# Kernel tuning notes

Hardware: AMD Instinct MI355X
Metric: run time of the kernel (lower is better)

Reference implementation:

```python
import jax, jax.numpy as jnp
import numpy as np

N = 21  # nodes per graph (20 laser sectors + 1 robot node)
MAX_RANGE = 10.0
_bound = np.linspace(-np.pi / 2 - 0.03, np.pi / 2, 21, dtype=np.float32)[:-1]
_angles = _bound + np.float32(np.pi / 20)
ANGLE_FEAT = jnp.asarray(np.stack([np.sin(_angles), np.cos(_angles)], 1), dtype=jnp.float32)  # [20,2]


def _build_nodes(state24):
    # state24: [B,24] -> node features [B,21,7]
    B = state24.shape[0]
    laser = state24[:, :20, None] / MAX_RANGE                       # [B,20,1]
    angle = jnp.broadcast_to(ANGLE_FEAT[None], (B, 20, 2))          # [B,20,2]
    sector = jnp.concatenate([laser, angle, jnp.zeros((B, 20, 4), state24.dtype)], -1)  # [B,20,7]
    robot = jnp.concatenate([jnp.zeros((B, 1, 3), state24.dtype), state24[:, None, 20:]], -1)  # [B,1,7]
    return jnp.concatenate([sector, robot], axis=1)                 # [B,21,7]


def _gatv2(x, Wl, Wr, att, bias, heads, dim):
    # GATv2 over a fully-connected graph with self-loops (dense all-pairs).
    # e_ij = att . leaky_relu(Wl x_j + Wr x_i); alpha = softmax_j; out_i = sum_j alpha_ij (Wl x_j)
    B = x.shape[0]
    gl = (x @ Wl).reshape(B, N, heads, dim)  # source transform [B,j,H,D]
    gr = (x @ Wr).reshape(B, N, heads, dim)  # target transform [B,i,H,D]
    s = jax.nn.leaky_relu(gl[:, None] + gr[:, :, None], negative_slope=0.2)  # [B,i,j,H,D]
    e = jnp.einsum('bijhd,hd->bijh', s, att)                                  # [B,i,j,H]
    alpha = jax.nn.softmax(e, axis=2)                                          # softmax over sources j
    out = jnp.einsum('bijh,bjhd->bihd', alpha, gl).reshape(B, N, heads * dim)
    return out + bias


def setup_inputs() -> dict:
    key = jax.random.key(0)
    ks = jax.random.split(key, 16)
    r = lambda k, shape, s: (jax.random.normal(k, shape, dtype=jnp.float32) * s)
    B = 1024
    return {
        'state24': jax.random.normal(ks[0], (B, 24), dtype=jnp.float32),
        'Wl1': r(ks[1], (7, 256), 0.3), 'Wr1': r(ks[2], (7, 256), 0.3),
        'att1': r(ks[3], (4, 64), 0.1), 'b1': r(ks[4], (256,), 0.02),
        'Wl2': r(ks[5], (256, 64), 0.06), 'Wr2': r(ks[6], (256, 64), 0.06),
        'att2': r(ks[7], (1, 64), 0.1), 'b2': r(ks[8], (64,), 0.02),
        'fc1_w': r(ks[9], (64, 256), 0.12), 'fc1_b': r(ks[10], (256,), 0.02),
        'fc2_w': r(ks[11], (256, 256), 0.06), 'fc2_b': r(ks[12], (256,), 0.02),
        'fc3_w': r(ks[13], (256, 2), 0.06), 'fc3_b': r(ks[14], (2,), 0.02),
    }


def reference(state24, Wl1, Wr1, att1, b1, Wl2, Wr2, att2, b2,
              fc1_w, fc1_b, fc2_w, fc2_b, fc3_w, fc3_b):
    x = _build_nodes(state24)                               # [B,21,7]
    h = jax.nn.elu(_gatv2(x, Wl1, Wr1, att1, b1, 4, 64))    # [B,21,256]
    h = _gatv2(h, Wl2, Wr2, att2, b2, 1, 64)                # [B,21,64]
    nfv = jnp.mean(h, axis=1)                               # global_mean_pool -> [B,64]
    h = jax.nn.relu(nfv @ fc1_w + fc1_b)
    h = jax.nn.relu(h @ fc2_w + fc2_b)
    return jnp.tanh(h @ fc3_w + fc3_b)                      # [B,2]
```

## Files before the change

### kernel.cpp

```cpp
#include <hip/hip_runtime.h>
#include <hip/hip_fp16.h>
#include <math.h>

#define PI_D 3.141592653589793

typedef _Float16 h2 __attribute__((ext_vector_type(2)));
typedef _Float16 h4 __attribute__((ext_vector_type(4)));
typedef _Float16 h8 __attribute__((ext_vector_type(8)));
typedef unsigned short us8 __attribute__((ext_vector_type(8)));
typedef __fp16 f16v2 __attribute__((ext_vector_type(2)));
typedef __fp16 f16v8 __attribute__((ext_vector_type(8)));
typedef float f32x4 __attribute__((ext_vector_type(4)));

#define STR1 264
#define STR2H 72

#define SV(v, a, b) __builtin_shufflevector(v, v, a, b)

static __device__ __forceinline__ h2 pack_h2(float a, float b) {
    return __builtin_bit_cast(h2, __builtin_amdgcn_cvt_pkrtz(a, b));
}

static __device__ __forceinline__ float fdot2(h2 a, h2 b, float c) {
    return __builtin_amdgcn_fdot2(__builtin_bit_cast(f16v2, a),
                                  __builtin_bit_cast(f16v2, b), c, false);
}

static __device__ __forceinline__ h8 habs8(h8 x) {
    us8 u = __builtin_bit_cast(us8, x);
    us8 m = {0x7fff, 0x7fff, 0x7fff, 0x7fff, 0x7fff, 0x7fff, 0x7fff, 0x7fff};
    return __builtin_bit_cast(h8, (us8)(u & m));
}

static __device__ __forceinline__ f32x4 mfma16(h8 a, h8 b, f32x4 c) {
    return __builtin_amdgcn_mfma_f32_16x16x32_f16(
        __builtin_bit_cast(f16v8, a), __builtin_bit_cast(f16v8, b), c, 0, 0, 0);
}

static __device__ __forceinline__ void wave_fence() {
    asm volatile("" ::: "memory");
#if __has_builtin(__builtin_amdgcn_wave_barrier)
    __builtin_amdgcn_wave_barrier();
#endif
    asm volatile("" ::: "memory");
}

__global__ __launch_bounds__(256) void pack_weights_kernel(
    const float* __restrict__ Wl2, const float* __restrict__ Wr2,
    const float* __restrict__ fc1_w, const float* __restrict__ fc2_w,
    h8* __restrict__ ws)
{
    int idx = blockIdx.x * 256 + threadIdx.x;
    if (idx < 4096) {
        const float* W = idx < 2048 ? Wl2 : Wr2;
        int t = idx & 2047;
        int ntile = t >> 9, rem = t & 511;
        int kchunk = rem >> 6, lane = rem & 63;
        int n = ntile * 16 + (lane & 15);
        int k0 = kchunk * 32 + (lane >> 4) * 8;
        h8 o;
        #pragma unroll
        for (int j = 0; j < 8; ++j) o[j] = (_Float16)W[(k0 + j) * 64 + n];
        ws[idx] = o;
    } else if (idx < 6144) {
        int t = idx - 4096;
        int k2 = t >> 6, c = t & 63;
        h8 o;
        #pragma unroll
        for (int q = 0; q < 4; ++q) {
            o[2 * q]     = (_Float16)fc1_w[(2 * k2) * 256 + 4 * c + q];
            o[2 * q + 1] = (_Float16)fc1_w[(2 * k2 + 1) * 256 + 4 * c + q];
        }
        ws[idx] = o;
    } else {
        int t = idx - 6144;
        int k2 = t >> 6, c = t & 63;
        h8 o;
        #pragma unroll
        for (int q = 0; q < 4; ++q) {
            o[2 * q]     = (_Float16)fc2_w[(2 * k2) * 256 + 4 * c + q];
            o[2 * q + 1] = (_Float16)fc2_w[(2 * k2 + 1) * 256 + 4 * c + q];
        }
        ws[idx] = o;
    }
}

__global__ __launch_bounds__(256, 2) void actor_fused_kernel(
    const float* __restrict__ state24,
    const float* __restrict__ Wl1, const float* __restrict__ Wr1,
    const float* __restrict__ att1, const float* __restrict__ b1,
    const float* __restrict__ att2, const float* __restrict__ b2,
    const float* __restrict__ fc1_b, const float* __restrict__ fc2_b,
    const float* __restrict__ fc3_w, const float* __restrict__ fc3_b,
    const h8* __restrict__ wsL, const h8* __restrict__ wsR,
    const h8* __restrict__ wsF1, const h8* __restrict__ wsF2,
    float* __restrict__ out, int B)
{
    const int bix = blockIdx.x;
    const int tid = threadIdx.x;
    const int smp0 = 2 * bix;
    if (smp0 >= B) return;
    const int smp1 = (smp0 + 1 < B) ? smp0 + 1 : smp0;

    __shared__ float sinL[20], cosL[20], laserL[2][20], robotL[2][4];
    __shared__ __align__(16) h2 attLh[128];
    __shared__ __align__(16) h2 att2Lh[32];
    __shared__ __align__(16) _Float16 gr1h[2][22 * STR1];
    __shared__ __align__(16) union {
        struct { _Float16 gl1h[2][22 * STR1];
                 float ePf[2][128 * 24];
                 float uv[2][168]; } p1;
        struct { _Float16 gl2h[2][21 * STR2H];
                 _Float16 gr2h[2][21 * STR2H];
                 _Float16 gl2hT[2][64 * 32];
                 float e2[2][32 * 24];
                 float u2v2[2][42];
                 float red[2][4][256];
                 _Float16 nfvh[2][64]; _Float16 hah[2][256]; _Float16 hbh[2][256]; } p2;
    } U;

    if (tid < 20) {
        double step = (PI_D + 0.03) / 20.0;
        float bound = (float)(-PI_D / 2.0 - 0.03 + (double)tid * step);
        float ang = bound + (float)(PI_D / 20.0);
        sinL[tid] = sinf(ang);
        cosL[tid] = cosf(ang);
        laserL[0][tid] = state24[smp0 * 24 + tid] * 0.1f;
        laserL[1][tid] = state24[smp1 * 24 + tid] * 0.1f;
    }
    if (tid >= 32 && tid < 40) {
        int s = (tid - 32) >> 2, q = (tid - 32) & 3;
        robotL[s][q] = state24[(s ? smp1 : smp0) * 24 + 20 + q];
    }
    if (tid < 128) {
        float2 ap = ((const float2*)att1)[tid];
        attLh[tid] = pack_h2(0.4f * ap.x, 0.4f * ap.y);
    }
    if (tid >= 128 && tid < 160) {
        float2 ap = ((const float2*)att2)[tid - 128];
        att2Lh[tid - 128] = pack_h2(0.4f * ap.x, 0.4f * ap.y);
    }
    __syncthreads();

    {
        const int h = tid >> 6;
        const int lane = tid & 63;

        {
            const int cp = lane & 31;
            const int half = lane >> 5;
            const int d2 = h * 32 + cp;
            float2 wl[7], wr[7];
            #pragma unroll
            for (int k = 0; k < 7; k++) {
                wl[k] = ((const float2*)Wl1)[k * 128 + d2];
                wr[k] = ((const float2*)Wr1)[k * 128 + d2];
            }
            if (half == 0) {
                h2 zz2 = {};
                #pragma unroll
                for (int s = 0; s < 2; ++s) {
                    ((h2*)(U.p1.gl1h[s] + 21 * STR1))[d2] = zz2;
                    ((h2*)(gr1h[s] + 21 * STR1))[d2] = zz2;
                }
            }
            const int base = half * 11;
            #pragma unroll
            for (int nn = 0; nn < 11; ++nn) {
                int node = base + nn;
                if (node < 21) {
                    #pragma unroll
                    for (int s = 0; s < 2; ++s) {
                        float a0, a1, b0, b1v;
                        if (node < 20) {
                            float l = laserL[s][node], sv = sinL[node], c = cosL[node];
                            a0 = l * wl[0].x + sv * wl[1].x + c * wl[2].x;
                            a1 = l * wl[0].y + sv * wl[1].y + c * wl[2].y;
                            b0 = l * wr[0].x + sv * wr[1].x + c * wr[2].x;
                            b1v = l * wr[0].y + sv * wr[1].y + c * wr[2].y;
                        } else {
                            float r0 = robotL[s][0], r1 = robotL[s][1], r2 = robotL[s][2], r3 = robotL[s][3];
                            a0 = r0 * wl[3].x + r1 * wl[4].x + r2 * wl[5].x + r3 * wl[6].x;
                            a1 = r0 * wl[3].y + r1 * wl[4].y + r2 * wl[5].y + r3 * wl[6].y;
                            b0 = r0 * wr[3].x + r1 * wr[4].x + r2 * wr[5].x + r3 * wr[6].x;
                            b1v = r0 * wr[3].y + r1 * wr[4].y + r2 * wr[5].y + r3 * wr[6].y;
                        }
                        ((h2*)(U.p1.gl1h[s] + node * STR1))[d2] = pack_h2(a0, a1);
                        ((h2*)(gr1h[s] + node * STR1))[d2] = pack_h2(b0, b1v);
                    }
                }
            }
        }
        wave_fence();

        {
            h2 ar[32];
            #pragma unroll
            for (int q = 0; q < 32; ++q) ar[q] = attLh[h * 32 + q];

            const bool act = lane < 63;
            const int jn  = act ? lane % 21 : 0;
            const int seg = act ? lane / 21 : 0;

            #pragma unroll
            for (int s = 0; s < 2; ++s) {
                const h8* gA8 = (const h8*)(U.p1.gl1h[s] + jn * STR1 + h * 64);
                h8 gj[8];
                #pragma unroll
                for (int ch = 0; ch < 8; ++ch) gj[ch] = gA8[ch];

                if (act && seg == 0) {
                    float l0 = 0.f, l1 = 0.f;
                    #pragma unroll
                    for (int ch = 0; ch < 8; ++ch) {
                        l0 = fdot2(SV(gj[ch], 0, 1), ar[ch * 4 + 0], l0);
                        l1 = fdot2(SV(gj[ch], 2, 3), ar[ch * 4 + 1], l1);
                        l0 = fdot2(SV(gj[ch], 4, 5), ar[ch * 4 + 2], l0);
                        l1 = fdot2(SV(gj[ch], 6, 7), ar[ch * 4 + 3], l1);
                    }
                    U.p1.uv[s][h * 21 + jn] = l0 + l1;
                }

                #pragma unroll
                for (int t = 0; t < 7; ++t) {
                    const int i = seg * 7 + t;
                    const h8* gB8 = (const h8*)(gr1h[s] + i * STR1 + h * 64);
                    float m0 = 0.f, m1 = 0.f;
                    #pragma unroll
                    for (int ch = 0; ch < 8; ++ch) {
                        h8 x = gj[ch] + gB8[ch];
                        h8 ax = habs8(x);
                        m0 = fdot2(SV(ax, 0, 1), ar[ch * 4 + 0], m0);
                        m1 = fdot2(SV(ax, 2, 3), ar[ch * 4 + 1], m1);
                        m0 = fdot2(SV(ax, 4, 5), ar[ch * 4 + 2], m0);
                        m1 = fdot2(SV(ax, 6, 7), ar[ch * 4 + 3], m1);
                    }
                    if (act) U.p1.ePf[s][(h * 32 + i) * 24 + jn] = m0 + m1;
                }
            }

            if (lane < 42) {
                const int s = lane >= 21;
                const int idx = lane - s * 21;
                const h8* row8 = (const h8*)(gr1h[s] + idx * STR1 + h * 64);
                float l0 = 0.f, l1 = 0.f;
                #pragma unroll
                for (int ch = 0; ch < 8; ++ch) {
                    h8 g = row8[ch];
                    l0 = fdot2(SV(g, 0, 1), ar[ch * 4 + 0], l0);
                    l1 = fdot2(SV(g, 2, 3), ar[ch * 4 + 1], l1);
                    l0 = fdot2(SV(g, 4, 5), ar[ch * 4 + 2], l0);
                    l1 = fdot2(SV(g, 6, 7), ar[ch * 4 + 3], l1);
                }
                U.p1.uv[s][84 + h * 21 + idx] = l0 + l1;
            }
        }
        wave_fence();

        if (lane < 42) {
            int s = lane >= 21;
            int i = lane - s * 21;
            int r = h * 32 + i;
            float* row = U.p1.ePf[s] + r * 24;
            const float* uu = U.p1.uv[s] + h * 21;
            float vi = 1.5f * U.p1.uv[s][84 + h * 21 + i];
            float ebuf[21];
            float m = -1e30f;
            #pragma unroll
            for (int j = 0; j < 21; j++) {
                float e = row[j] + 1.5f * uu[j] + vi;
                ebuf[j] = e;
                m = fmaxf(m, e);
            }
            float sum = 0.f;
            #pragma unroll
            for (int j = 0; j < 21; j++) { float v = __expf(ebuf[j] - m); ebuf[j] = v; sum += v; }
            float rinv = 1.f / sum;
            h8* hp8 = (h8*)(U.p1.ePf[s]) + r * 6;
            h8 o0, o1, o2;
            #pragma unroll
            for (int q = 0; q < 8; ++q) o0[q] = (_Float16)(ebuf[q] * rinv);
            #pragma unroll
            for (int q = 0; q < 8; ++q) o1[q] = (_Float16)(ebuf[8 + q] * rinv);
            #pragma unroll
            for (int q = 0; q < 5; ++q) o2[q] = (_Float16)(ebuf[16 + q] * rinv);
            o2[5] = (_Float16)0.f; o2[6] = (_Float16)0.f; o2[7] = (_Float16)0.f;
            h8 zz = {};
            hp8[0] = o0; hp8[1] = o1; hp8[2] = o2;
            hp8[3] = zz; hp8[4] = zz; hp8[5] = zz;
        }
        {
            h8 zz = {};
            for (int z = lane; z < 132; z += 64) {
                int s = z >= 66;
                int zz2 = z - s * 66;
                int rr = zz2 / 6, slot = zz2 - rr * 6;
                ((h8*)U.p1.ePf[s])[(h * 32 + 21 + rr) * 6 + slot] = zz;
            }
        }
        wave_fence();

        {
            const int mcol = lane & 15;
            const int quad = lane >> 4;
            h8 A0s[2], A1s[2];
            #pragma unroll
            for (int s = 0; s < 2; ++s) {
                const h8* Af = (const h8*)U.p1.ePf[s];
                A0s[s] = Af[(h * 32 + mcol) * 6 + quad];
                A1s[s] = Af[(h * 32 + 16 + mcol) * 6 + quad];
            }
            int rowoff[8];
            #pragma unroll
            for (int jj = 0; jj < 8; ++jj) {
                int rr = quad * 8 + jj;
                rowoff[jj] = (rr > 21 ? 21 : rr) * STR1;
            }
            const int colbase = h * 64 + mcol;
            f32x4 z4 = {0.f, 0.f, 0.f, 0.f};
            #pragma unroll
            for (int t = 0; t < 4; ++t) {
                int col = colbase + t * 16;
                float bb = b1[col];
                #pragma unroll
                for (int s = 0; s < 2; ++s) {
                    h8 bv;
                    #pragma unroll
                    for (int jj = 0; jj < 8; ++jj) bv[jj] = U.p1.gl1h[s][rowoff[jj] + col];
                    f32x4 d0 = mfma16(A0s[s], bv, z4);
                    f32x4 d1 = mfma16(A1s[s], bv, z4);
                    #pragma unroll
                    for (int r = 0; r < 4; ++r) {
                        int n0 = quad * 4 + r;
                        float v = d0[r] + bb;
                        v = v > 0.f ? v : __expf(v) - 1.f;
                        gr1h[s][n0 * STR1 + col] = (_Float16)v;
                        int n1 = 16 + quad * 4 + r;
                        if (n1 < 21) {
                            float w2 = d1[r] + bb;
                            w2 = w2 > 0.f ? w2 : __expf(w2) - 1.f;
                            gr1h[s][n1 * STR1 + col] = (_Float16)w2;
                        }
                    }
                }
            }
        }
    }
    __syncthreads();

    {
        const int lane = tid & 63;
        const int w = tid >> 6;
        const int mrow = lane & 15;
        const int quad = lane >> 4;
        int rowA1 = 16 + mrow; if (rowA1 > 21) rowA1 = 21;
        const h8* bL = wsL + w * 512 + lane;
        const h8* bR = wsR + w * 512 + lane;
        f32x4 aL0[2], aL1[2], aR0[2], aR1[2];
        #pragma unroll
        for (int s = 0; s < 2; ++s) {
            aL0[s] = (f32x4){0.f, 0.f, 0.f, 0.f}; aL1[s] = (f32x4){0.f, 0.f, 0.f, 0.f};
            aR0[s] = (f32x4){0.f, 0.f, 0.f, 0.f}; aR1[s] = (f32x4){0.f, 0.f, 0.f, 0.f};
        }
        #pragma unroll
        for (int kc = 0; kc < 8; ++kc) {
            h8 BL = bL[kc * 64];
            h8 BR = bR[kc * 64];
            #pragma unroll
            for (int s = 0; s < 2; ++s) {
                h8 A0 = *(const h8*)(gr1h[s] + mrow * STR1 + quad * 8 + kc * 32);
                h8 A1 = *(const h8*)(gr1h[s] + rowA1 * STR1 + quad * 8 + kc * 32);
                aL0[s] = mfma16(A0, BL, aL0[s]);
                aL1[s] = mfma16(A1, BL, aL1[s]);
                aR0[s] = mfma16(A0, BR, aR0[s]);
                aR1[s] = mfma16(A1, BR, aR1[s]);
            }
        }
        const int col = w * 16 + mrow;
        #pragma unroll
        for (int s = 0; s < 2; ++s) {
            #pragma unroll
            for (int r = 0; r < 4; ++r) {
                int row0 = quad * 4 + r;
                U.p2.gl2h[s][row0 * STR2H + col] = (_Float16)aL0[s][r];
                U.p2.gr2h[s][row0 * STR2H + col] = (_Float16)aR0[s][r];
                int row1 = 16 + row0;
                if (row1 < 21) {
                    U.p2.gl2h[s][row1 * STR2H + col] = (_Float16)aL1[s][r];
                    U.p2.gr2h[s][row1 * STR2H + col] = (_Float16)aR1[s][r];
                }
            }
            h2 lo0 = pack_h2(aL0[s][0], aL0[s][1]);
            h2 hi0 = pack_h2(aL0[s][2], aL0[s][3]);
            h4 p0 = __builtin_shufflevector(lo0, hi0, 0, 1, 2, 3);
            *(h4*)(U.p2.gl2hT[s] + col * 32 + quad * 4) = p0;
            h2 lo1 = pack_h2(aL1[s][0], aL1[s][1]);
            h2 hi1 = pack_h2(aL1[s][2], aL1[s][3]);
            h4 p1 = __builtin_shufflevector(lo1, hi1, 0, 1, 2, 3);
            *(h4*)(U.p2.gl2hT[s] + col * 32 + 16 + quad * 4) = p1;
        }
    }
    __syncthreads();

    {
        h2 ar2[32];
        #pragma unroll
        for (int q = 0; q < 32; ++q) ar2[q] = att2Lh[q];

        const bool act = tid < 252;
        const int t0 = act ? tid : 0;
        const int jn = t0 % 21;
        const int sg = (t0 / 21) % 6;
        const int s  = t0 / 126;

        const h8* gA8 = (const h8*)(U.p2.gl2h[s] + jn * STR2H);
        h8 gj[8];
        #pragma unroll
        for (int ch = 0; ch < 8; ++ch) gj[ch] = gA8[ch];

        if (act && sg == 0) {
            float l0 = 0.f, l1 = 0.f;
            #pragma unroll
            for (int ch = 0; ch < 8; ++ch) {
                l0 = fdot2(SV(gj[ch], 0, 1), ar2[ch * 4 + 0], l0);
                l1 = fdot2(SV(gj[ch], 2, 3), ar2[ch * 4 + 1], l1);
                l0 = fdot2(SV(gj[ch], 4, 5), ar2[ch * 4 + 2], l0);
                l1 = fdot2(SV(gj[ch], 6, 7), ar2[ch * 4 + 3], l1);
            }
            U.p2.u2v2[s][jn] = l0 + l1;
        }

        #pragma unroll
        for (int tt = 0; tt < 4; ++tt) {
            const int i = sg * 4 + tt;
            const int ri = i < 21 ? i : 20;
            const h8* gB8 = (const h8*)(U.p2.gr2h[s] + ri * STR2H);
            float m0 = 0.f, m1 = 0.f;
            #pragma unroll
            for (int ch = 0; ch < 8; ++ch) {
                h8 x = gj[ch] + gB8[ch];
                h8 ax = habs8(x);
                m0 = fdot2(SV(ax, 0, 1), ar2[ch * 4 + 0], m0);
                m1 = fdot2(SV(ax, 2, 3), ar2[ch * 4 + 1], m1);
                m0 = fdot2(SV(ax, 4, 5), ar2[ch * 4 + 2], m0);
                m1 = fdot2(SV(ax, 6, 7), ar2[ch * 4 + 3], m1);
            }
            if (act && i < 21) U.p2.e2[s][i * 24 + jn] = m0 + m1;
        }

        if (tid < 42) {
            const int ss = tid >= 21;
            const int idx = tid - ss * 21;
            const h8* row8 = (const h8*)(U.p2.gr2h[ss] + idx * STR2H);
            float l0 = 0.f, l1 = 0.f;
            #pragma unroll
            for (int ch = 0; ch < 8; ++ch) {
                h8 g = row8[ch];
                l0 = fdot2(SV(g, 0, 1), ar2[ch * 4 + 0], l0);
                l1 = fdot2(SV(g, 2, 3), ar2[ch * 4 + 1], l1);
                l0 = fdot2(SV(g, 4, 5), ar2[ch * 4 + 2], l0);
                l1 = fdot2(SV(g, 6, 7), ar2[ch * 4 + 3], l1);
            }
            U.p2.u2v2[ss][21 + idx] = l0 + l1;
        }
    }
    __syncthreads();

    if (tid < 42) {
        int s = tid >= 21;
        int i = tid - s * 21;
        float* row = U.p2.e2[s] + i * 24;
        const float* uu = U.p2.u2v2[s];
        float vi = 1.5f * U.p2.u2v2[s][21 + i];
        float ebuf[21];
        float m = -1e30f;
        #pragma unroll
        for (int j = 0; j < 21; j++) {
            float e = row[j] + 1.5f * uu[j] + vi;
            ebuf[j] = e;
            m = fmaxf(m, e);
        }
        float sum = 0.f;
        #pragma unroll
        for (int j = 0; j < 21; j++) { float v = __expf(ebuf[j] - m); ebuf[j] = v; sum += v; }
        float rinv = 1.f / sum;
        h8* hp8 = (h8*)(U.p2.e2[s]) + i * 6;
        h8 o0, o1, o2;
        #pragma unroll
        for (int q = 0; q < 8; ++q) o0[q] = (_Float16)(ebuf[q] * rinv);
        #pragma unroll
        for (int q = 0; q < 8; ++q) o1[q] = (_Float16)(ebuf[8 + q] * rinv);
        #pragma unroll
        for (int q = 0; q < 5; ++q) o2[q] = (_Float16)(ebuf[16 + q] * rinv);
        o2[5] = (_Float16)0.f; o2[6] = (_Float16)0.f; o2[7] = (_Float16)0.f;
        h8 zz = {};
        hp8[0] = o0; hp8[1] = o1; hp8[2] = o2;
        hp8[3] = zz; hp8[4] = zz; hp8[5] = zz;
    } else if (tid < 174) {
        int z = tid - 42;
        int s = z >= 66;
        int zz2 = z - s * 66;
        int rr = zz2 / 6, slot = zz2 - rr * 6;
        h8 zz = {};
        ((h8*)U.p2.e2[s])[(21 + rr) * 6 + slot] = zz;
    }
    __syncthreads();

    {
        const int lane = tid & 63;
        const int w = tid >> 6;
        const int mcol = lane & 15;
        const int quad = lane >> 4;
        const int col = w * 16 + mcol;
        float bb = b2[col];
        f32x4 z4 = {0.f, 0.f, 0.f, 0.f};
        #pragma unroll
        for (int s = 0; s < 2; ++s) {
            const h8* Af2 = (const h8*)U.p2.e2[s];
            h8 A0 = Af2[mcol * 6 + quad];
            h8 A1 = Af2[(16 + mcol) * 6 + quad];
            h8 bv = *(const h8*)(U.p2.gl2hT[s] + col * 32 + quad * 8);
            f32x4 d0 = mfma16(A0, bv, z4);
            f32x4 d1 = mfma16(A1, bv, z4);
            float sum = (d0[0] + d0[1]) + (d0[2] + d0[3])
                      + (d1[0] + d1[1]) + (d1[2] + d1[3]);
            sum += __shfl_xor(sum, 16, 64);
            sum += __shfl_xor(sum, 32, 64);
            if (quad == 0) U.p2.nfvh[s][col] = (_Float16)(sum * (1.f / 21.f) + bb);
        }
    }
    __syncthreads();

    {
        int c = tid & 63, g = tid >> 6;
        float4 acc0 = {0.f, 0.f, 0.f, 0.f}, acc1 = {0.f, 0.f, 0.f, 0.f};
        #pragma unroll
        for (int kk = 0; kk < 8; ++kk) {
            int k2 = g * 8 + kk;
            h8 w = wsF1[k2 * 64 + c];
            h2 x0 = ((const h2*)U.p2.nfvh[0])[k2];
            h2 x1 = ((const h2*)U.p2.nfvh[1])[k2];
            acc0.x = fdot2(SV(w, 0, 1), x0, acc0.x);
            acc0.y = fdot2(SV(w, 2, 3), x0, acc0.y);
            acc0.z = fdot2(SV(w, 4, 5), x0, acc0.z);
            acc0.w = fdot2(SV(w, 6, 7), x0, acc0.w);
            acc1.x = fdot2(SV(w, 0, 1), x1, acc1.x);
            acc1.y = fdot2(SV(w, 2, 3), x1, acc1.y);
            acc1.z = fdot2(SV(w, 4, 5), x1, acc1.z);
            acc1.w = fdot2(SV(w, 6, 7), x1, acc1.w);
        }
        ((float4*)U.p2.red[0][g])[c] = acc0;
        ((float4*)U.p2.red[1][g])[c] = acc1;
    }
    __syncthreads();
    {
        float bb = fc1_b[tid];
        #pragma unroll
        for (int s = 0; s < 2; ++s) {
            float v = U.p2.red[s][0][tid] + U.p2.red[s][1][tid]
                    + U.p2.red[s][2][tid] + U.p2.red[s][3][tid] + bb;
            U.p2.hah[s][tid] = (_Float16)fmaxf(v, 0.f);
        }
    }
    __syncthreads();

    {
        int c = tid & 63, g = tid >> 6;
        const h8* ha0 = (const h8*)U.p2.hah[0];
        const h8* ha1 = (const h8*)U.p2.hah[1];
        float4 acc0 = {0.f, 0.f, 0.f, 0.f}, acc1 = {0.f, 0.f, 0.f, 0.f};
#define FC2_STEP(q, p)                                                          \
        {                                                                       \
            int k2 = g * 32 + (q) * 4 + (p);                                    \
            h8 w = wsF2[k2 * 64 + c];                                           \
            h2 x0 = __builtin_shufflevector(xa0, xa0, 2 * (p), 2 * (p) + 1);    \
            h2 x1 = __builtin_shufflevector(xa1, xa1, 2 * (p), 2 * (p) + 1);    \
            acc0.x = fdot2(SV(w, 0, 1), x0, acc0.x);                            \
            acc0.y = fdot2(SV(w, 2, 3), x0, acc0.y);                            \
            acc0.z = fdot2(SV(w, 4, 5), x0, acc0.z);                            \
            acc0.w = fdot2(SV(w, 6, 7), x0, acc0.w);                            \
            acc1.x = fdot2(SV(w, 0, 1), x1, acc1.x);                            \
            acc1.y = fdot2(SV(w, 2, 3), x1, acc1.y);                            \
            acc1.z = fdot2(SV(w, 4, 5), x1, acc1.z);                            \
            acc1.w = fdot2(SV(w, 6, 7), x1, acc1.w);                            \
        }
        #pragma unroll
        for (int q = 0; q < 8; ++q) {
            h8 xa0 = ha0[g * 8 + q];
            h8 xa1 = ha1[g * 8 + q];
            FC2_STEP(q, 0)
            FC2_STEP(q, 1)
            FC2_STEP(q, 2)
            FC2_STEP(q, 3)
        }
#undef FC2_STEP
        ((float4*)U.p2.red[0][g])[c] = acc0;
        ((float4*)U.p2.red[1][g])[c] = acc1;
    }
    __syncthreads();
    {
        float bb = fc2_b[tid];
        #pragma unroll
        for (int s = 0; s < 2; ++s) {
            float v = U.p2.red[s][0][tid] + U.p2.red[s][1][tid]
                    + U.p2.red[s][2][tid] + U.p2.red[s][3][tid] + bb;
            U.p2.hbh[s][tid] = (_Float16)fmaxf(v, 0.f);
        }
    }
    __syncthreads();

    {
        int g = tid >> 6;
        int o = g & 1, s = g >> 1;
        int l = tid & 63;
        float sum = 0.f;
        #pragma unroll
        for (int m = 0; m < 4; m++) {
            int k = l + 64 * m;
            sum = fmaf((float)U.p2.hbh[s][k], fc3_w[k * 2 + o], sum);
        }
        #pragma unroll
        for (int off = 32; off >= 1; off >>= 1) sum += __shfl_down(sum, off, 64);
        if (l == 0 && smp0 + s < B) out[(smp0 + s) * 2 + o] = tanhf(sum + fc3_b[o]);
    }
}

extern "C" void kernel_launch(void* const* d_in, const int* in_sizes, int n_in,
                              void* d_out, int out_size, void* d_ws, size_t ws_size,
                              hipStream_t stream) {
    const float* state24 = (const float*)d_in[0];
    const float* Wl1 = (const float*)d_in[1];
    const float* Wr1 = (const float*)d_in[2];
    const float* att1 = (const float*)d_in[3];
    const float* b1 = (const float*)d_in[4];
    const float* Wl2 = (const float*)d_in[5];
    const float* Wr2 = (const float*)d_in[6];
    const float* att2 = (const float*)d_in[7];
    const float* b2 = (const float*)d_in[8];
    const float* fc1_w = (const float*)d_in[9];
    const float* fc1_b = (const float*)d_in[10];
    const float* fc2_w = (const float*)d_in[11];
    const float* fc2_b = (const float*)d_in[12];
    const float* fc3_w = (const float*)d_in[13];
    const float* fc3_b = (const float*)d_in[14];
    float* out = (float*)d_out;

    h8* ws = (h8*)d_ws;
    const h8* wsL = ws;
    const h8* wsR = ws + 2048;
    const h8* wsF1 = ws + 4096;
    const h8* wsF2 = ws + 6144;

    pack_weights_kernel<<<56, 256, 0, stream>>>(Wl2, Wr2, fc1_w, fc2_w, ws);

    int B = in_sizes[0] / 24;
    int nb = (B + 1) / 2;
    actor_fused_kernel<<<nb, 256, 0, stream>>>(
        state24, Wl1, Wr1, att1, b1, att2, b2,
        fc1_b, fc2_b, fc3_w, fc3_b,
        wsL, wsR, wsF1, wsF2, out, B);
}
```

Baseline: 112.7 us.

## Process one sample per block instead of two to raise occupancy

```diff
diff --git a/kernel.cpp b/kernel.cpp
--- a/kernel.cpp
+++ b/kernel.cpp
@@ -85,7 +85,7 @@
     }
 }
 
-__global__ __launch_bounds__(256, 2) void actor_fused_kernel(
+__global__ __launch_bounds__(256, 4) void actor_fused_kernel(
     const float* __restrict__ state24,
     const float* __restrict__ Wl1, const float* __restrict__ Wr1,
     const float* __restrict__ att1, const float* __restrict__ b1,
@@ -96,27 +96,24 @@
     const h8* __restrict__ wsF1, const h8* __restrict__ wsF2,
     float* __restrict__ out, int B)
 {
-    const int bix = blockIdx.x;
+    const int smp = blockIdx.x;
     const int tid = threadIdx.x;
-    const int smp0 = 2 * bix;
-    if (smp0 >= B) return;
-    const int smp1 = (smp0 + 1 < B) ? smp0 + 1 : smp0;
-
-    __shared__ float sinL[20], cosL[20], laserL[2][20], robotL[2][4];
+
+    __shared__ float sinL[20], cosL[20], laserL[20], robotL[4];
     __shared__ __align__(16) h2 attLh[128];
     __shared__ __align__(16) h2 att2Lh[32];
-    __shared__ __align__(16) _Float16 gr1h[2][22 * STR1];
+    __shared__ __align__(16) _Float16 gr1h[22 * STR1];
     __shared__ __align__(16) union {
-        struct { _Float16 gl1h[2][22 * STR1];
-                 float ePf[2][128 * 24];
-                 float uv[2][168]; } p1;
-        struct { _Float16 gl2h[2][21 * STR2H];
-                 _Float16 gr2h[2][21 * STR2H];
-                 _Float16 gl2hT[2][64 * 32];
-                 float e2[2][32 * 24];
-                 float u2v2[2][42];
-                 float red[2][4][256];
-                 _Float16 nfvh[2][64]; _Float16 hah[2][256]; _Float16 hbh[2][256]; } p2;
+        struct { _Float16 gl1h[22 * STR1];
+                 float ePf[128 * 24];
+                 float uv[168]; } p1;
+        struct { _Float16 gl2h[21 * STR2H];
+                 _Float16 gr2h[21 * STR2H];
+                 _Float16 gl2hT[64 * 32];
+                 float e2[32 * 24];
+                 float u2v2[42];
+                 float red[4][256];
+                 _Float16 nfvh[64]; _Float16 hah[256]; _Float16 hbh[256]; } p2;
     } U;
 
     if (tid < 20) {
@@ -125,12 +122,11 @@
         float ang = bound + (float)(PI_D / 20.0);
         sinL[tid] = sinf(ang);
         cosL[tid] = cosf(ang);
-        laserL[0][tid] = state24[smp0 * 24 + tid] * 0.1f;
-        laserL[1][tid] = state24[smp1 * 24 + tid] * 0.1f;
-    }
-    if (tid >= 32 && tid < 40) {
-        int s = (tid - 32) >> 2, q = (tid - 32) & 3;
-        robotL[s][q] = state24[(s ? smp1 : smp0) * 24 + 20 + q];
+        laserL[tid] = state24[smp * 24 + tid] * 0.1f;
+    }
+    if (tid >= 32 && tid < 36) {
+        int q = tid - 32;
+        robotL[q] = state24[smp * 24 + 20 + q];
     }
     if (tid < 128) {
         float2 ap = ((const float2*)att1)[tid];
@@ -158,36 +154,30 @@
             }
             if (half == 0) {
                 h2 zz2 = {};
-                #pragma unroll
-                for (int s = 0; s < 2; ++s) {
-                    ((h2*)(U.p1.gl1h[s] + 21 * STR1))[d2] = zz2;
-                    ((h2*)(gr1h[s] + 21 * STR1))[d2] = zz2;
-                }
+                ((h2*)(U.p1.gl1h + 21 * STR1))[d2] = zz2;
+                ((h2*)(gr1h + 21 * STR1))[d2] = zz2;
             }
             const int base = half * 11;
             #pragma unroll
             for (int nn = 0; nn < 11; ++nn) {
                 int node = base + nn;
                 if (node < 21) {
-                    #pragma unroll
-                    for (int s = 0; s < 2; ++s) {
-                        float a0, a1, b0, b1v;
-                        if (node < 20) {
-                            float l = laserL[s][node], sv = sinL[node], c = cosL[node];
-                            a0 = l * wl[0].x + sv * wl[1].x + c * wl[2].x;
-                            a1 = l * wl[0].y + sv * wl[1].y + c * wl[2].y;
-                            b0 = l * wr[0].x + sv * wr[1].x + c * wr[2].x;
-                            b1v = l * wr[0].y + sv * wr[1].y + c * wr[2].y;
-                        } else {
-                            float r0 = robotL[s][0], r1 = robotL[s][1], r2 = robotL[s][2], r3 = robotL[s][3];
-                            a0 = r0 * wl[3].x + r1 * wl[4].x + r2 * wl[5].x + r3 * wl[6].x;
-                            a1 = r0 * wl[3].y + r1 * wl[4].y + r2 * wl[5].y + r3 * wl[6].y;
-                            b0 = r0 * wr[3].x + r1 * wr[4].x + r2 * wr[5].x + r3 * wr[6].x;
-                            b1v = r0 * wr[3].y + r1 * wr[4].y + r2 * wr[5].y + r3 * wr[6].y;
-                        }
-                        ((h2*)(U.p1.gl1h[s] + node * STR1))[d2] = pack_h2(a0, a1);
-                        ((h2*)(gr1h[s] + node * STR1))[d2] = pack_h2(b0, b1v);
+                    float a0, a1, b0, b1v;
+                    if (node < 20) {
+                        float l = laserL[node], sv = sinL[node], c = cosL[node];
+                        a0 = l * wl[0].x + sv * wl[1].x + c * wl[2].x;
+                        a1 = l * wl[0].y + sv * wl[1].y + c * wl[2].y;
+                        b0 = l * wr[0].x + sv * wr[1].x + c * wr[2].x;
+                        b1v = l * wr[0].y + sv * wr[1].y + c * wr[2].y;
+                    } else {
+                        float r0 = robotL[0], r1 = robotL[1], r2 = robotL[2], r3 = robotL[3];
+                        a0 = r0 * wl[3].x + r1 * wl[4].x + r2 * wl[5].x + r3 * wl[6].x;
+                        a1 = r0 * wl[3].y + r1 * wl[4].y + r2 * wl[5].y + r3 * wl[6].y;
+                        b0 = r0 * wr[3].x + r1 * wr[4].x + r2 * wr[5].x + r3 * wr[6].x;
+                        b1v = r0 * wr[3].y + r1 * wr[4].y + r2 * wr[5].y + r3 * wr[6].y;
                     }
+                    ((h2*)(U.p1.gl1h + node * STR1))[d2] = pack_h2(a0, a1);
+                    ((h2*)(gr1h + node * STR1))[d2] = pack_h2(b0, b1v);
                 }
             }
         }
@@ -202,47 +192,42 @@
             const int jn  = act ? lane % 21 : 0;
             const int seg = act ? lane / 21 : 0;
 
-            #pragma unroll
-            for (int s = 0; s < 2; ++s) {
-                const h8* gA8 = (const h8*)(U.p1.gl1h[s] + jn * STR1 + h * 64);
-                h8 gj[8];
+            const h8* gA8 = (const h8*)(U.p1.gl1h + jn * STR1 + h * 64);
+            h8 gj[8];
+            #pragma unroll
+            for (int ch = 0; ch < 8; ++ch) gj[ch] = gA8[ch];
+
+            if (act && seg == 0) {
+                float l0 = 0.f, l1 = 0.f;
                 #pragma unroll
-                for (int ch = 0; ch < 8; ++ch) gj[ch] = gA8[ch];
-
-                if (act && seg == 0) {
-                    float l0 = 0.f, l1 = 0.f;
-                    #pragma unroll
-                    for (int ch = 0; ch < 8; ++ch) {
-                        l0 = fdot2(SV(gj[ch], 0, 1), ar[ch * 4 + 0], l0);
-                        l1 = fdot2(SV(gj[ch], 2, 3), ar[ch * 4 + 1], l1);
-                        l0 = fdot2(SV(gj[ch], 4, 5), ar[ch * 4 + 2], l0);
-                        l1 = fdot2(SV(gj[ch], 6, 7), ar[ch * 4 + 3], l1);
-                    }
-                    U.p1.uv[s][h * 21 + jn] = l0 + l1;
+                for (int ch = 0; ch < 8; ++ch) {
+                    l0 = fdot2(SV(gj[ch], 0, 1), ar[ch * 4 + 0], l0);
+                    l1 = fdot2(SV(gj[ch], 2, 3), ar[ch * 4 + 1], l1);
+                    l0 = fdot2(SV(gj[ch], 4, 5), ar[ch * 4 + 2], l0);
+                    l1 = fdot2(SV(gj[ch], 6, 7), ar[ch * 4 + 3], l1);
                 }
-
+                U.p1.uv[h * 21 + jn] = l0 + l1;
+            }
+
+            #pragma unroll
+            for (int t = 0; t < 7; ++t) {
+                const int i = seg * 7 + t;
+                const h8* gB8 = (const h8*)(gr1h + i * STR1 + h * 64);
+                float m0 = 0.f, m1 = 0.f;
                 #pragma unroll
-                for (int t = 0; t < 7; ++t) {
-                    const int i = seg * 7 + t;
-                    const h8* gB8 = (const h8*)(gr1h[s] + i * STR1 + h * 64);
-                    float m0 = 0.f, m1 = 0.f;
-                    #pragma unroll
-                    for (int ch = 0; ch < 8; ++ch) {
-                        h8 x = gj[ch] + gB8[ch];
-                        h8 ax = habs8(x);
-                        m0 = fdot2(SV(ax, 0, 1), ar[ch * 4 + 0], m0);
-                        m1 = fdot2(SV(ax, 2, 3), ar[ch * 4 + 1], m1);
-                        m0 = fdot2(SV(ax, 4, 5), ar[ch * 4 + 2], m0);
-                        m1 = fdot2(SV(ax, 6, 7), ar[ch * 4 + 3], m1);
-                    }
-                    if (act) U.p1.ePf[s][(h * 32 + i) * 24 + jn] = m0 + m1;
+                for (int ch = 0; ch < 8; ++ch) {
+                    h8 x = gj[ch] + gB8[ch];
+                    h8 ax = habs8(x);
+                    m0 = fdot2(SV(ax, 0, 1), ar[ch * 4 + 0], m0);
+                    m1 = fdot2(SV(ax, 2, 3), ar[ch * 4 + 1], m1);
+                    m0 = fdot2(SV(ax, 4, 5), ar[ch * 4 + 2], m0);
+                    m1 = fdot2(SV(ax, 6, 7), ar[ch * 4 + 3], m1);
                 }
-            }
-
-            if (lane < 42) {
-                const int s = lane >= 21;
-                const int idx = lane - s * 21;
-                const h8* row8 = (const h8*)(gr1h[s] + idx * STR1 + h * 64);
+                if (act) U.p1.ePf[(h * 32 + i) * 24 + jn] = m0 + m1;
+            }
+
+            if (lane < 21) {
+                const h8* row8 = (const h8*)(gr1h + lane * STR1 + h * 64);
                 float l0 = 0.f, l1 = 0.f;
                 #pragma unroll
                 for (int ch = 0; ch < 8; ++ch) {
@@ -252,18 +237,17 @@
                     l0 = fdot2(SV(g, 4, 5), ar[ch * 4 + 2], l0);
                     l1 = fdot2(SV(g, 6, 7), ar[ch * 4 + 3], l1);
                 }
-                U.p1.uv[s][84 + h * 21 + idx] = l0 + l1;
+                U.p1.uv[84 + h * 21 + lane] = l0 + l1;
             }
         }
         wave_fence();
 
-        if (lane < 42) {
-            int s = lane >= 21;
-            int i = lane - s * 21;
+        if (lane < 21) {
+            int i = lane;
             int r = h * 32 + i;
-            float* row = U.p1.ePf[s] + r * 24;
-            const float* uu = U.p1.uv[s] + h * 21;
-            float vi = 1.5f * U.p1.uv[s][84 + h * 21 + i];
+            float* row = U.p1.ePf + r * 24;
+            const float* uu = U.p1.uv + h * 21;
+            float vi = 1.5f * U.p1.uv[84 + h * 21 + i];
             float ebuf[21];
             float m = -1e30f;
             #pragma unroll
@@ -276,7 +260,7 @@
             #pragma unroll
             for (int j = 0; j < 21; j++) { float v = __expf(ebuf[j] - m); ebuf[j] = v; sum += v; }
             float rinv = 1.f / sum;
-            h8* hp8 = (h8*)(U.p1.ePf[s]) + r * 6;
+            h8* hp8 = (h8*)(U.p1.ePf) + r * 6;
             h8 o0, o1, o2;
             #pragma unroll
             for (int q = 0; q < 8; ++q) o0[q] = (_Float16)(ebuf[q] * rinv);
@@ -291,11 +275,9 @@
         }
         {
             h8 zz = {};
-            for (int z = lane; z < 132; z += 64) {
-                int s = z >= 66;
-                int zz2 = z - s * 66;
-                int rr = zz2 / 6, slot = zz2 - rr * 6;
-                ((h8*)U.p1.ePf[s])[(h * 32 + 21 + rr) * 6 + slot] = zz;
+            for (int z = lane; z < 66; z += 64) {
+                int rr = z / 6, slot = z - rr * 6;
+                ((h8*)U.p1.ePf)[(h * 32 + 21 + rr) * 6 + slot] = zz;
             }
         }
         wave_fence();
@@ -303,13 +285,9 @@
         {
             const int mcol = lane & 15;
             const int quad = lane >> 4;
-            h8 A0s[2], A1s[2];
-            #pragma unroll
-            for (int s = 0; s < 2; ++s) {
-                const h8* Af = (const h8*)U.p1.ePf[s];
-                A0s[s] = Af[(h * 32 + mcol) * 6 + quad];
-                A1s[s] = Af[(h * 32 + 16 + mcol) * 6 + quad];
-            }
+            const h8* Af = (const h8*)U.p1.ePf;
+            h8 A0 = Af[(h * 32 + mcol) * 6 + quad];
+            h8 A1 = Af[(h * 32 + 16 + mcol) * 6 + quad];
             int rowoff[8];
             #pragma unroll
             for (int jj = 0; jj < 8; ++jj) {
@@ -322,25 +300,22 @@
             for (int t = 0; t < 4; ++t) {
                 int col = colbase + t * 16;
                 float bb = b1[col];
+                h8 bv;
                 #pragma unroll
-                for (int s = 0; s < 2; ++s) {
-                    h8 bv;
-                    #pragma unroll
-                    for (int jj = 0; jj < 8; ++jj) bv[jj] = U.p1.gl1h[s][rowoff[jj] + col];
-                    f32x4 d0 = mfma16(A0s[s], bv, z4);
-                    f32x4 d1 = mfma16(A1s[s], bv, z4);
-                    #pragma unroll
-                    for (int r = 0; r < 4; ++r) {
-                        int n0 = quad * 4 + r;
-                        float v = d0[r] + bb;
-                        v = v > 0.f ? v : __expf(v) - 1.f;
-                        gr1h[s][n0 * STR1 + col] = (_Float16)v;
-                        int n1 = 16 + quad * 4 + r;
-                        if (n1 < 21) {
-                            float w2 = d1[r] + bb;
-                            w2 = w2 > 0.f ? w2 : __expf(w2) - 1.f;
-                            gr1h[s][n1 * STR1 + col] = (_Float16)w2;
-                        }
+                for (int jj = 0; jj < 8; ++jj) bv[jj] = U.p1.gl1h[rowoff[jj] + col];
+                f32x4 d0 = mfma16(A0, bv, z4);
+                f32x4 d1 = mfma16(A1, bv, z4);
+                #pragma unroll
+                for (int r = 0; r < 4; ++r) {
+                    int n0 = quad * 4 + r;
+                    float v = d0[r] + bb;
+                    v = v > 0.f ? v : __expf(v) - 1.f;
+                    gr1h[n0 * STR1 + col] = (_Float16)v;
+                    int n1 = 16 + quad * 4 + r;
+                    if (n1 < 21) {
+                        float w2 = d1[r] + bb;
+                        w2 = w2 > 0.f ? w2 : __expf(w2) - 1.f;
+                        gr1h[n1 * STR1 + col] = (_Float16)w2;
                     }
                 }
             }
@@ -356,49 +331,39 @@
         int rowA1 = 16 + mrow; if (rowA1 > 21) rowA1 = 21;
         const h8* bL = wsL + w * 512 + lane;
         const h8* bR = wsR + w * 512 + lane;
-        f32x4 aL0[2], aL1[2], aR0[2], aR1[2];
-        #pragma unroll
-        for (int s = 0; s < 2; ++s) {
-            aL0[s] = (f32x4){0.f, 0.f, 0.f, 0.f}; aL1[s] = (f32x4){0.f, 0.f, 0.f, 0.f};
-            aR0[s] = (f32x4){0.f, 0.f, 0.f, 0.f}; aR1[s] = (f32x4){0.f, 0.f, 0.f, 0.f};
-        }
+        f32x4 aL0 = {0.f, 0.f, 0.f, 0.f}, aL1 = {0.f, 0.f, 0.f, 0.f};
+        f32x4 aR0 = {0.f, 0.f, 0.f, 0.f}, aR1 = {0.f, 0.f, 0.f, 0.f};
         #pragma unroll
         for (int kc = 0; kc < 8; ++kc) {
             h8 BL = bL[kc * 64];
             h8 BR = bR[kc * 64];
-            #pragma unroll
-            for (int s = 0; s < 2; ++s) {
-                h8 A0 = *(const h8*)(gr1h[s] + mrow * STR1 + quad * 8 + kc * 32);
-                h8 A1 = *(const h8*)(gr1h[s] + rowA1 * STR1 + quad * 8 + kc * 32);
-                aL0[s] = mfma16(A0, BL, aL0[s]);
-                aL1[s] = mfma16(A1, BL, aL1[s]);
-                aR0[s] = mfma16(A0, BR, aR0[s]);
-                aR1[s] = mfma16(A1, BR, aR1[s]);
-            }
+            h8 A0 = *(const h8*)(gr1h + mrow * STR1 + quad * 8 + kc * 32);
+            h8 A1 = *(const h8*)(gr1h + rowA1 * STR1 + quad * 8 + kc * 32);
+            aL0 = mfma16(A0, BL, aL0);
+            aL1 = mfma16(A1, BL, aL1);
+            aR0 = mfma16(A0, BR, aR0);
+            aR1 = mfma16(A1, BR, aR1);
         }
         const int col = w * 16 + mrow;
         #pragma unroll
-        for (int s = 0; s < 2; ++s) {
-            #pragma unroll
-            for (int r = 0; r < 4; ++r) {
-                int row0 = quad * 4 + r;
-                U.p2.gl2h[s][row0 * STR2H + col] = (_Float16)aL0[s][r];
-                U.p2.gr2h[s][row0 * STR2H + col] = (_Float16)aR0[s][r];
-                int row1 = 16 + row0;
-                if (row1 < 21) {
-                    U.p2.gl2h[s][row1 * STR2H + col] = (_Float16)aL1[s][r];
-                    U.p2.gr2h[s][row1 * STR2H + col] = (_Float16)aR1[s][r];
-                }
-            }
-            h2 lo0 = pack_h2(aL0[s][0], aL0[s][1]);
-            h2 hi0 = pack_h2(aL0[s][2], aL0[s][3]);
-            h4 p0 = __builtin_shufflevector(lo0, hi0, 0, 1, 2, 3);
-            *(h4*)(U.p2.gl2hT[s] + col * 32 + quad * 4) = p0;
-            h2 lo1 = pack_h2(aL1[s][0], aL1[s][1]);
-            h2 hi1 = pack_h2(aL1[s][2], aL1[s][3]);
-            h4 p1 = __builtin_shufflevector(lo1, hi1, 0, 1, 2, 3);
-            *(h4*)(U.p2.gl2hT[s] + col * 32 + 16 + quad * 4) = p1;
-        }
+        for (int r = 0; r < 4; ++r) {
+            int row0 = quad * 4 + r;
+            U.p2.gl2h[row0 * STR2H + col] = (_Float16)aL0[r];
+            U.p2.gr2h[row0 * STR2H + col] = (_Float16)aR0[r];
+            int row1 = 16 + row0;
+            if (row1 < 21) {
+                U.p2.gl2h[row1 * STR2H + col] = (_Float16)aL1[r];
+                U.p2.gr2h[row1 * STR2H + col] = (_Float16)aR1[r];
+            }
+        }
+        h2 lo0 = pack_h2(aL0[0], aL0[1]);
+        h2 hi0 = pack_h2(aL0[2], aL0[3]);
+        h4 p0 = __builtin_shufflevector(lo0, hi0, 0, 1, 2, 3);
+        *(h4*)(U.p2.gl2hT + col * 32 + quad * 4) = p0;
+        h2 lo1 = pack_h2(aL1[0], aL1[1]);
+        h2 hi1 = pack_h2(aL1[2], aL1[3]);
+        h4 p1 = __builtin_shufflevector(lo1, hi1, 0, 1, 2, 3);
+        *(h4*)(U.p2.gl2hT + col * 32 + 16 + quad * 4) = p1;
     }
     __syncthreads();
 
@@ -410,10 +375,9 @@
         const bool act = tid < 252;
         const int t0 = act ? tid : 0;
         const int jn = t0 % 21;
-        const int sg = (t0 / 21) % 6;
-        const int s  = t0 / 126;
-
-        const h8* gA8 = (const h8*)(U.p2.gl2h[s] + jn * STR2H);
+        const int sg = t0 / 21;
+
+        const h8* gA8 = (const h8*)(U.p2.gl2h + jn * STR2H);
         h8 gj[8];
         #pragma unroll
         for (int ch = 0; ch < 8; ++ch) gj[ch] = gA8[ch];
@@ -427,31 +391,29 @@
                 l0 = fdot2(SV(gj[ch], 4, 5), ar2[ch * 4 + 2], l0);
                 l1 = fdot2(SV(gj[ch], 6, 7), ar2[ch * 4 + 3], l1);
             }
-            U.p2.u2v2[s][jn] = l0 + l1;
-        }
-
-        #pragma unroll
-        for (int tt = 0; tt < 4; ++tt) {
-            const int i = sg * 4 + tt;
-            const int ri = i < 21 ? i : 20;
-            const h8* gB8 = (const h8*)(U.p2.gr2h[s] + ri * STR2H);
-            float m0 = 0.f, m1 = 0.f;
-            #pragma unroll
-            for (int ch = 0; ch < 8; ++ch) {
-                h8 x = gj[ch] + gB8[ch];
-                h8 ax = habs8(x);
-                m0 = fdot2(SV(ax, 0, 1), ar2[ch * 4 + 0], m0);
-                m1 = fdot2(SV(ax, 2, 3), ar2[ch * 4 + 1], m1);
-                m0 = fdot2(SV(ax, 4, 5), ar2[ch * 4 + 2], m0);
-                m1 = fdot2(SV(ax, 6, 7), ar2[ch * 4 + 3], m1);
-            }
-            if (act && i < 21) U.p2.e2[s][i * 24 + jn] = m0 + m1;
-        }
-
-        if (tid < 42) {
-            const int ss = tid >= 21;
-            const int idx = tid - ss * 21;
-            const h8* row8 = (const h8*)(U.p2.gr2h[ss] + idx * STR2H);
+            U.p2.u2v2[jn] = l0 + l1;
+        }
+
+        if (sg < 11) {
+            #pragma unroll
+            for (int tt = 0; tt < 2; ++tt) {
+                const int i = sg * 2 + tt;
+                const int ri = i < 21 ? i : 20;
+                const h8* gB8 = (const h8*)(U.p2.gr2h + ri * STR2H);
+                float m0 = 0.f, m1 = 0.f;
+                #pragma unroll
+                for (int ch = 0; ch < 8; ++ch) {
+                    h8 x = gj[ch] + gB8[ch];
+                    h8 ax = habs8(x);
+                    m0 = fdot2(SV(ax, 0, 1), ar2[ch * 4 + 0], m0);
+                    m1 = fdot2(SV(ax, 2, 3), ar2[ch * 4 + 1], m1);
+                    m0 = fdot2(SV(ax, 4, 5), ar2[ch * 4 + 2], m0);
+                    m1 = fdot2(SV(ax, 6, 7), ar2[ch * 4 + 3], m1);
+                }
+                if (act && i < 21) U.p2.e2[i * 24 + jn] = m0 + m1;
+            }
+        } else if (act) {
+            const h8* row8 = (const h8*)(U.p2.gr2h + jn * STR2H);
             float l0 = 0.f, l1 = 0.f;
             #pragma unroll
             for (int ch = 0; ch < 8; ++ch) {
@@ -461,17 +423,16 @@
                 l0 = fdot2(SV(g, 4, 5), ar2[ch * 4 + 2], l0);
                 l1 = fdot2(SV(g, 6, 7), ar2[ch * 4 + 3], l1);
             }
-            U.p2.u2v2[ss][21 + idx] = l0 + l1;
-        }
-    }
-    __syncthreads();
-
-    if (tid < 42) {
-        int s = tid >= 21;
-        int i = tid - s * 21;
-        float* row = U.p2.e2[s] + i * 24;
-        const float* uu = U.p2.u2v2[s];
-        float vi = 1.5f * U.p2.u2v2[s][21 + i];
+            U.p2.u2v2[21 + jn] = l0 + l1;
+        }
+    }
+    __syncthreads();
+
+    if (tid < 21) {
+        int i = tid;
+        float* row = U.p2.e2 + i * 24;
+        const float* uu = U.p2.u2v2;
+        float vi = 1.5f * U.p2.u2v2[21 + i];
         float ebuf[21];
         float m = -1e30f;
         #pragma unroll
@@ -484,7 +445,7 @@
         #pragma unroll
         for (int j = 0; j < 21; j++) { float v = __expf(ebuf[j] - m); ebuf[j] = v; sum += v; }
         float rinv = 1.f / sum;
-        h8* hp8 = (h8*)(U.p2.e2[s]) + i * 6;
+        h8* hp8 = (h8*)(U.p2.e2) + i * 6;
         h8 o0, o1, o2;
         #pragma unroll
         for (int q = 0; q < 8; ++q) o0[q] = (_Float16)(ebuf[q] * rinv);
@@ -496,13 +457,11 @@
         h8 zz = {};
         hp8[0] = o0; hp8[1] = o1; hp8[2] = o2;
         hp8[3] = zz; hp8[4] = zz; hp8[5] = zz;
-    } else if (tid < 174) {
-        int z = tid - 42;
-        int s = z >= 66;
-        int zz2 = z - s * 66;
-        int rr = zz2 / 6, slot = zz2 - rr * 6;
+    } else if (tid < 87) {
+        int z = tid - 21;
+        int rr = z / 6, slot = z - rr * 6;
         h8 zz = {};
-        ((h8*)U.p2.e2[s])[(21 + rr) * 6 + slot] = zz;
+        ((h8*)U.p2.e2)[(21 + rr) * 6 + slot] = zz;
     }
     __syncthreads();
 
@@ -514,114 +473,93 @@
         const int col = w * 16 + mcol;
         float bb = b2[col];
         f32x4 z4 = {0.f, 0.f, 0.f, 0.f};
-        #pragma unroll
-        for (int s = 0; s < 2; ++s) {
-            const h8* Af2 = (const h8*)U.p2.e2[s];
-            h8 A0 = Af2[mcol * 6 + quad];
-            h8 A1 = Af2[(16 + mcol) * 6 + quad];
-            h8 bv = *(const h8*)(U.p2.gl2hT[s] + col * 32 + quad * 8);
-            f32x4 d0 = mfma16(A0, bv, z4);
-            f32x4 d1 = mfma16(A1, bv, z4);
-            float sum = (d0[0] + d0[1]) + (d0[2] + d0[3])
-                      + (d1[0] + d1[1]) + (d1[2] + d1[3]);
-            sum += __shfl_xor(sum, 16, 64);
-            sum += __shfl_xor(sum, 32, 64);
-            if (quad == 0) U.p2.nfvh[s][col] = (_Float16)(sum * (1.f / 21.f) + bb);
-        }
+        const h8* Af2 = (const h8*)U.p2.e2;
+        h8 A0 = Af2[mcol * 6 + quad];
+        h8 A1 = Af2[(16 + mcol) * 6 + quad];
+        h8 bv = *(const h8*)(U.p2.gl2hT + col * 32 + quad * 8);
+        f32x4 d0 = mfma16(A0, bv, z4);
+        f32x4 d1 = mfma16(A1, bv, z4);
+        float sum = (d0[0] + d0[1]) + (d0[2] + d0[3])
+                  + (d1[0] + d1[1]) + (d1[2] + d1[3]);
+        sum += __shfl_xor(sum, 16, 64);
+        sum += __shfl_xor(sum, 32, 64);
+        if (quad == 0) U.p2.nfvh[col] = (_Float16)(sum * (1.f / 21.f) + bb);
     }
     __syncthreads();
 
     {
         int c = tid & 63, g = tid >> 6;
-        float4 acc0 = {0.f, 0.f, 0.f, 0.f}, acc1 = {0.f, 0.f, 0.f, 0.f};
+        float4 acc = {0.f, 0.f, 0.f, 0.f};
         #pragma unroll
         for (int kk = 0; kk < 8; ++kk) {
             int k2 = g * 8 + kk;
             h8 w = wsF1[k2 * 64 + c];
-            h2 x0 = ((const h2*)U.p2.nfvh[0])[k2];
-            h2 x1 = ((const h2*)U.p2.nfvh[1])[k2];
-            acc0.x = fdot2(SV(w, 0, 1), x0, acc0.x);
-            acc0.y = fdot2(SV(w, 2, 3), x0, acc0.y);
-            acc0.z = fdot2(SV(w, 4, 5), x0, acc0.z);
-            acc0.w = fdot2(SV(w, 6, 7), x0, acc0.w);
-            acc1.x = fdot2(SV(w, 0, 1), x1, acc1.x);
-            acc1.y = fdot2(SV(w, 2, 3), x1, acc1.y);
-            acc1.z = fdot2(SV(w, 4, 5), x1, acc1.z);
-            acc1.w = fdot2(SV(w, 6, 7), x1, acc1.w);
-        }
-        ((float4*)U.p2.red[0][g])[c] = acc0;
-        ((float4*)U.p2.red[1][g])[c] = acc1;
+            h2 x = ((const h2*)U.p2.nfvh)[k2];
+            acc.x = fdot2(SV(w, 0, 1), x, acc.x);
+            acc.y = fdot2(SV(w, 2, 3), x, acc.y);
+            acc.z = fdot2(SV(w, 4, 5), x, acc.z);
+            acc.w = fdot2(SV(w, 6, 7), x, acc.w);
+        }
+        ((float4*)U.p2.red[g])[c] = acc;
     }
     __syncthreads();
     {
         float bb = fc1_b[tid];
-        #pragma unroll
-        for (int s = 0; s < 2; ++s) {
-            float v = U.p2.red[s][0][tid] + U.p2.red[s][1][tid]
-                    + U.p2.red[s][2][tid] + U.p2.red[s][3][tid] + bb;
-            U.p2.hah[s][tid] = (_Float16)fmaxf(v, 0.f);
-        }
+        float v = U.p2.red[0][tid] + U.p2.red[1][tid]
+                + U.p2.red[2][tid] + U.p2.red[3][tid] + bb;
+        U.p2.hah[tid] = (_Float16)fmaxf(v, 0.f);
     }
     __syncthreads();
 
     {
         int c = tid & 63, g = tid >> 6;
-        const h8* ha0 = (const h8*)U.p2.hah[0];
-        const h8* ha1 = (const h8*)U.p2.hah[1];
-        float4 acc0 = {0.f, 0.f, 0.f, 0.f}, acc1 = {0.f, 0.f, 0.f, 0.f};
+        const h8* ha = (const h8*)U.p2.hah;
+        float4 acc = {0.f, 0.f, 0.f, 0.f};
 #define FC2_STEP(q, p)                                                          \
         {                                                                       \
             int k2 = g * 32 + (q) * 4 + (p);                                    \
             h8 w = wsF2[k2 * 64 + c];                                           \
-            h2 x0 = __builtin_shufflevector(xa0, xa0, 2 * (p), 2 * (p) + 1);    \
-            h2 x1 = __builtin_shufflevector(xa1, xa1, 2 * (p), 2 * (p) + 1);    \
-            acc0.x = fdot2(SV(w, 0, 1), x0, acc0.x);                            \
-            acc0.y = fdot2(SV(w, 2, 3), x0, acc0.y);                            \
-            acc0.z = fdot2(SV(w, 4, 5), x0, acc0.z);                            \
-            acc0.w = fdot2(SV(w, 6, 7), x0, acc0.w);                            \
-            acc1.x = fdot2(SV(w, 0, 1), x1, acc1.x);                            \
-            acc1.y = fdot2(SV(w, 2, 3), x1, acc1.y);                            \
-            acc1.z = fdot2(SV(w, 4, 5), x1, acc1.z);                            \
-            acc1.w = fdot2(SV(w, 6, 7), x1, acc1.w);                            \
+            h2 x = __builtin_shufflevector(xa, xa, 2 * (p), 2 * (p) + 1);       \
+            acc.x = fdot2(SV(w, 0, 1), x, acc.x);                               \
+            acc.y = fdot2(SV(w, 2, 3), x, acc.y);                               \
+            acc.z = fdot2(SV(w, 4, 5), x, acc.z);                               \
+            acc.w = fdot2(SV(w, 6, 7), x, acc.w);                               \
         }
         #pragma unroll
         for (int q = 0; q < 8; ++q) {
-            h8 xa0 = ha0[g * 8 + q];
-            h8 xa1 = ha1[g * 8 + q];
+            h8 xa = ha[g * 8 + q];
             FC2_STEP(q, 0)
             FC2_STEP(q, 1)
             FC2_STEP(q, 2)
             FC2_STEP(q, 3)
         }
 #undef FC2_STEP
-        ((float4*)U.p2.red[0][g])[c] = acc0;
-        ((float4*)U.p2.red[1][g])[c] = acc1;
+        ((float4*)U.p2.red[g])[c] = acc;
     }
     __syncthreads();
     {
         float bb = fc2_b[tid];
-        #pragma unroll
-        for (int s = 0; s < 2; ++s) {
-            float v = U.p2.red[s][0][tid] + U.p2.red[s][1][tid]
-                    + U.p2.red[s][2][tid] + U.p2.red[s][3][tid] + bb;
-            U.p2.hbh[s][tid] = (_Float16)fmaxf(v, 0.f);
-        }
+        float v = U.p2.red[0][tid] + U.p2.red[1][tid]
+                + U.p2.red[2][tid] + U.p2.red[3][tid] + bb;
+        U.p2.hbh[tid] = (_Float16)fmaxf(v, 0.f);
     }
     __syncthreads();
 
     {
         int g = tid >> 6;
-        int o = g & 1, s = g >> 1;
-        int l = tid & 63;
-        float sum = 0.f;
-        #pragma unroll
-        for (int m = 0; m < 4; m++) {
-            int k = l + 64 * m;
-            sum = fmaf((float)U.p2.hbh[s][k], fc3_w[k * 2 + o], sum);
-        }
-        #pragma unroll
-        for (int off = 32; off >= 1; off >>= 1) sum += __shfl_down(sum, off, 64);
-        if (l == 0 && smp0 + s < B) out[(smp0 + s) * 2 + o] = tanhf(sum + fc3_b[o]);
+        if (g < 2) {
+            int o = g;
+            int l = tid & 63;
+            float sum = 0.f;
+            #pragma unroll
+            for (int m = 0; m < 4; m++) {
+                int k = l + 64 * m;
+                sum = fmaf((float)U.p2.hbh[k], fc3_w[k * 2 + o], sum);
+            }
+            #pragma unroll
+            for (int off = 32; off >= 1; off >>= 1) sum += __shfl_down(sum, off, 64);
+            if (l == 0) out[smp * 2 + o] = tanhf(sum + fc3_b[o]);
+        }
     }
 }
 
@@ -654,8 +592,7 @@
     pack_weights_kernel<<<56, 256, 0, stream>>>(Wl2, Wr2, fc1_w, fc2_w, ws);
 
     int B = in_sizes[0] / 24;
-    int nb = (B + 1) / 2;
-    actor_fused_kernel<<<nb, 256, 0, stream>>>(
+    actor_fused_kernel<<<B, 256, 0, stream>>>(
         state24, Wl1, Wr1, att1, b1, att2, b2,
         fc1_b, fc2_b, fc3_w, fc3_b,
         wsL, wsR, wsF1, wsF2, out, B);
```

After: 112.9 us. Within noise of the previous version (+0.2%).
